# Kernel tuning notes

Measured on AMD Instinct MI355X. Metric: run time of the kernel, lower is better.

Reference implementation:

```python
import jax, jax.numpy as jnp
import numpy as np

N, H, W, PD, HID, NH = 2, 64, 64, 16, 128, 4
EPS = 1e-5


def _bn(x, g, b):
    # training-mode BatchNorm over (N, H, W) with biased variance, channels last
    m = jnp.mean(x, axis=(0, 1, 2), keepdims=True)
    v = jnp.var(x, axis=(0, 1, 2), keepdims=True)
    return (x - m) * jax.lax.rsqrt(v + EPS) * g + b


def _mha(x, in_w, in_b, out_w, out_b, nh):
    # torch nn.MultiheadAttention (batch_first) with packed qkv in_proj
    B, S, E = x.shape
    hd = E // nh
    q, k, v = jnp.split(x @ in_w.T + in_b, 3, axis=-1)
    def heads(t):
        return t.reshape(B, S, nh, hd).transpose(0, 2, 1, 3)  # B,nh,S,hd
    q, k, v = heads(q), heads(k), heads(v)
    a = jax.nn.softmax(jnp.einsum('bnqd,bnkd->bnqk', q, k) / np.float32(np.sqrt(hd)), axis=-1)
    o = jnp.einsum('bnqk,bnkd->bnqd', a, v).transpose(0, 2, 1, 3).reshape(B, S, E)
    return o @ out_w.T + out_b


def setup_inputs():
    key = jax.random.key(0)
    ks = jax.random.split(key, 32)
    def r(i, shape, s=0.1):
        return jax.random.normal(ks[i], shape, dtype=jnp.float32) * s
    mask = (jnp.arange(W) % 2) == 0  # alternating columns kept, M = W//2
    return {
        'kspace': jax.random.normal(ks[0], (N, 2, H, W), dtype=jnp.float32),
        'mask': mask,
        'pre_conv_w': r(1, (PD, 2), 0.5), 'pre_conv_b': r(2, (PD,)),
        'pre_pe_H': r(3, (H, PD)), 'pre_pe_W': r(4, (W, PD)),
        'res_conv1_w': r(5, (PD, PD), 0.2), 'res_conv1_b': r(6, (PD,)),
        'res_bn1_g': 1.0 + r(7, (PD,)), 'res_bn1_b': r(8, (PD,)),
        'res_conv2_w': r(9, (PD, PD), 0.2), 'res_conv2_b': r(10, (PD,)),
        'res_bn2_g': 1.0 + r(11, (PD,)), 'res_bn2_b': r(12, (PD,)),
        'proj_w': r(13, (HID, PD), 0.2), 'proj_b': r(14, (HID,)),
        'enc_in_w': r(15, (3 * HID, HID), 0.08), 'enc_in_b': r(16, (3 * HID,)),
        'enc_out_w': r(17, (HID, HID), 0.08), 'enc_out_b': r(18, (HID,)),
        'dec_pe_H': r(19, (H, HID)), 'dec_pe_W': r(20, (W, HID)),
        'dec_in_w': r(21, (3 * HID, HID), 0.08), 'dec_in_b': r(22, (3 * HID,)),
        'dec_out_w': r(23, (HID, HID), 0.08), 'dec_out_b': r(24, (HID,)),
        'masked_token': r(25, (HID,), 1.0),
        'post_w': r(26, (2, HID), 0.1), 'post_b': r(27, (2,)),
    }


def reference(kspace, mask, pre_conv_w, pre_conv_b, pre_pe_H, pre_pe_W,
              res_conv1_w, res_conv1_b, res_bn1_g, res_bn1_b,
              res_conv2_w, res_conv2_b, res_bn2_g, res_bn2_b,
              proj_w, proj_b, enc_in_w, enc_in_b, enc_out_w, enc_out_b,
              dec_pe_H, dec_pe_W, dec_in_w, dec_in_b, dec_out_w, dec_out_b,
              masked_token, post_w, post_b):
    cols = np.nonzero(np.asarray(mask))[0]  # static sampled columns
    M = cols.shape[0]
    # gather valid columns; channels last: [N, H, M, 2]
    x = kspace.transpose(0, 2, 3, 1)[:, :, cols, :]
    h = x @ pre_conv_w.T + pre_conv_b  # 1x1 conv -> [N, H, M, PD]
    h = h + (pre_pe_H[:, None, :] + pre_pe_W[cols][None, :, :])
    # PixelwiseConstantChannelResNet (1 layer)
    r1 = jax.nn.relu(_bn(h @ res_conv1_w.T + res_conv1_b, res_bn1_g, res_bn1_b))
    r2 = jax.nn.relu(_bn(r1 @ res_conv2_w.T + res_conv2_b, res_bn2_g, res_bn2_b))
    h = jax.nn.relu(h + r2)
    h = h @ proj_w.T + proj_b  # [N, H, M, HID]
    enc = _mha(h.reshape(N, H * M, HID), enc_in_w, enc_in_b, enc_out_w, enc_out_b, NH)
    # scatter: fill unmasked positions with masked_token, masked with encoder output
    dec = jnp.broadcast_to(masked_token, (N, H, W, HID))
    dec = dec.at[:, :, cols, :].set(enc.reshape(N, H, M, HID))
    dec = dec + (dec_pe_H[:, None, :] + dec_pe_W[None, :, :])
    dec = _mha(dec.reshape(N, H * W, HID), dec_in_w, dec_in_b, dec_out_w, dec_out_b, NH)
    out = dec.reshape(N, H, W, HID) @ post_w.T + post_b  # [N, H, W, 2]
    return out.transpose(0, 3, 1, 2)  # [N, 2, H, W]
```

## Files before the change

kernel.cpp:

```cpp
#include <hip/hip_runtime.h>
#include <math.h>

#define N_ 2
#define H_ 64
#define W_ 64
#define M_ 32
#define PD_ 16
#define HID_ 128
#define NH_ 4
#define HD_ 32
#define S_ENC 2048
#define S_DEC 4096
#define EPS_ 1e-5f
#define SCALE_ 0.17677669529663687f
#define SCALE2_ (0.17677669529663687f * 1.4426950408889634f)

#define OFF_H     0
#define OFF_T1    65536
#define OFF_T2    131072
#define OFF_STAT  196608
#define OFF_WP    196672
#define OFF_BP    202816
#define OFF_QBF   203264
#define OFF_KBF   727552
#define OFF_VTBF  1251840
#define OFF_ATTBF 1776128
#define OFF_XBF2  2300416
#define OFF_WBF   2824704

#define WOFF_ENC_OUT 0
#define WOFF_DEC_IN  16384
#define WOFF_DEC_OUT 65536

#define IB_MF   2048
#define IB_WC   320
#define IB_WP   24
#define IB_BP   2
#define IB_TOT  (IB_MF + IB_WC + IB_WP + IB_BP + 1)

typedef short bf16x8 __attribute__((ext_vector_type(8)));
typedef short bf16x4 __attribute__((ext_vector_type(4)));
typedef float f32x4 __attribute__((ext_vector_type(4)));

__device__ __forceinline__ short f2bf(float f) {
  union { float f; unsigned u; } v; v.f = f;
  unsigned r = v.u + 0x7FFFu + ((v.u >> 16) & 1u);
  return (short)(r >> 16);
}

__global__ void k_init(const float* __restrict__ eow, const float* __restrict__ dw,
                       const float* __restrict__ dow, const float* __restrict__ mt,
                       const float* __restrict__ peH, const float* __restrict__ peW,
                       const float* __restrict__ ew, const float* __restrict__ pw,
                       const float* __restrict__ pb, const float* __restrict__ eib,
                       short* __restrict__ wbf, short* __restrict__ xdec,
                       float* __restrict__ wp, float* __restrict__ bp,
                       float* __restrict__ stat) {
  int blk = blockIdx.x, tid = threadIdx.x;
  if (blk < IB_MF) {
    int idx = blk * 256 + tid;
    int j = idx & 127;
    int widx = (idx >> 7) & 31;
    int hh = (idx >> 12) & 63;
    int b = idx >> 18;
    int w = 2 * widx + 1;
    xdec[((size_t)(b * 4096 + hh * 64 + w)) * 128 + j] =
        f2bf(mt[j] + peH[hh * 128 + j] + peW[w * 128 + j]);
  } else if (blk < IB_MF + IB_WC) {
    int idx = (blk - IB_MF) * 256 + tid;
    float v;
    if (idx < 16384) v = eow[idx];
    else if (idx < 65536) v = dw[idx - 16384];
    else v = dow[idx - 65536];
    wbf[idx] = f2bf(v);
  } else if (blk < IB_MF + IB_WC + IB_WP) {
    int e = (blk - IB_MF - IB_WC) * 256 + tid;
    int row = e >> 4, k = e & 15;
    float a = 0.f;
    for (int j = 0; j < 128; j++) a = fmaf(ew[row * 128 + j], pw[j * 16 + k], a);
    wp[e] = a;
  } else if (blk < IB_MF + IB_WC + IB_WP + IB_BP) {
    int row = (blk - IB_MF - IB_WC - IB_WP) * 256 + tid;
    if (row < 384) {
      float a = eib[row];
      for (int j = 0; j < 128; j++) a = fmaf(ew[row * 128 + j], pb[j], a);
      bp[row] = a;
    }
  } else {
    if (tid < 64) stat[tid] = 0.f;
  }
}

__global__ void k_prelin_stats(const float* __restrict__ ks, const float* __restrict__ pcw,
                               const float* __restrict__ pcb, const float* __restrict__ peH,
                               const float* __restrict__ peW, const float* __restrict__ w1,
                               const float* __restrict__ b1, float* __restrict__ h,
                               float* __restrict__ t1, float* __restrict__ stat) {
  int tid = threadIdx.x;
  int pos = blockIdx.x * 256 + tid;
  int m = pos & 31, hh = (pos >> 5) & 63, b = pos >> 11;
  int w = 2 * m;
  float x0 = ks[((b * 2 + 0) * H_ + hh) * W_ + w];
  float x1 = ks[((b * 2 + 1) * H_ + hh) * W_ + w];
  float hv[16], tv[16];
#pragma unroll
  for (int c = 0; c < 16; c++)
    hv[c] = x0 * pcw[c * 2] + x1 * pcw[c * 2 + 1] + pcb[c]
            + peH[hh * PD_ + c] + peW[w * PD_ + c];
#pragma unroll
  for (int c = 0; c < 16; c += 4)
    *(float4*)&h[pos * 16 + c] = make_float4(hv[c], hv[c + 1], hv[c + 2], hv[c + 3]);
#pragma unroll
  for (int c = 0; c < 16; c++) {
    float a = b1[c];
#pragma unroll
    for (int k = 0; k < 16; k++) a = fmaf(hv[k], w1[c * 16 + k], a);
    tv[c] = a;
    t1[pos * 16 + c] = a;
  }
  __shared__ float tl[256][17];
#pragma unroll
  for (int c = 0; c < 16; c++) tl[tid][c] = tv[c];
  __syncthreads();
  int c = tid & 15, g = tid >> 4;
  float s = 0.f, s2 = 0.f;
#pragma unroll
  for (int r = 0; r < 16; r++) {
    float v = tl[g * 16 + r][c];
    s += v; s2 += v * v;
  }
  __shared__ float ps[16][16], ps2[16][16];
  ps[g][c] = s; ps2[g][c] = s2;
  __syncthreads();
  if (tid < 16) {
    float S = 0.f, S2 = 0.f;
#pragma unroll
    for (int g2 = 0; g2 < 16; g2++) { S += ps[g2][tid]; S2 += ps2[g2][tid]; }
    atomicAdd(&stat[tid], S);
    atomicAdd(&stat[16 + tid], S2);
  }
}

__global__ void k_bnlin_stats(const float* __restrict__ t1, const float* __restrict__ stat,
                              const float* __restrict__ g1, const float* __restrict__ bb1,
                              const float* __restrict__ w2, const float* __restrict__ b2,
                              float* __restrict__ t2, float* __restrict__ statw) {
  int tid = threadIdx.x;
  int pos = blockIdx.x * 256 + tid;
  const float inv = 1.f / 4096.f;
  float r[16];
#pragma unroll
  for (int k = 0; k < 16; k++) {
    float mu = stat[k] * inv;
    float var = stat[16 + k] * inv - mu * mu;
    float v = (t1[pos * 16 + k] - mu) * rsqrtf(var + EPS_) * g1[k] + bb1[k];
    r[k] = fmaxf(v, 0.f);
  }
  float tv[16];
#pragma unroll
  for (int c = 0; c < 16; c++) {
    float a = b2[c];
#pragma unroll
    for (int k = 0; k < 16; k++) a = fmaf(r[k], w2[c * 16 + k], a);
    tv[c] = a;
    t2[pos * 16 + c] = a;
  }
  __shared__ float tl[256][17];
#pragma unroll
  for (int c = 0; c < 16; c++) tl[tid][c] = tv[c];
  __syncthreads();
  int c = tid & 15, g = tid >> 4;
  float s = 0.f, s2 = 0.f;
#pragma unroll
  for (int rr = 0; rr < 16; rr++) {
    float v = tl[g * 16 + rr][c];
    s += v; s2 += v * v;
  }
  __shared__ float ps[16][16], ps2[16][16];
  ps[g][c] = s; ps2[g][c] = s2;
  __syncthreads();
  if (tid < 16) {
    float S = 0.f, S2 = 0.f;
#pragma unroll
    for (int g2 = 0; g2 < 16; g2++) { S += ps[g2][tid]; S2 += ps2[g2][tid]; }
    atomicAdd(&statw[32 + tid], S);
    atomicAdd(&statw[48 + tid], S2);
  }
}

__global__ __launch_bounds__(256)
void k_fqkv_enc(const float* __restrict__ h, const float* __restrict__ t2,
                const float* __restrict__ stat, const float* __restrict__ g2,
                const float* __restrict__ bb2, const float* __restrict__ wp,
                const float* __restrict__ bp, short* __restrict__ qbf,
                short* __restrict__ kbf, short* __restrict__ vtbf) {
  int tid = threadIdx.x;
  int p0 = blockIdx.x * 32;
  __shared__ float hf[32][20];
  const float inv = 1.f / 4096.f;
#pragma unroll
  for (int i = 0; i < 2; i++) {
    int idx = tid * 2 + i;
    int lp = idx >> 4, c = idx & 15;
    int pos = p0 + lp;
    float mu = stat[32 + c] * inv;
    float var = stat[48 + c] * inv - mu * mu;
    float v = (t2[pos * 16 + c] - mu) * rsqrtf(var + EPS_) * g2[c] + bb2[c];
    v = fmaxf(v, 0.f);
    hf[lp][c] = fmaxf(h[pos * 16 + c] + v, 0.f);
  }
  __syncthreads();
  int bb = p0 >> 11;
  int sbase = p0 & 2047;
  {
    int col = tid;
    float wc[16];
#pragma unroll
    for (int k = 0; k < 16; k += 4) *(float4*)&wc[k] = *(const float4*)&wp[col * 16 + k];
    float bpv = bp[col];
    int isQ = (col < 128);
    int c2 = isQ ? col : (col - 128);
    int hd = c2 >> 5, d = c2 & 31;
    short* dst = isQ ? qbf : kbf;
    float sc = isQ ? SCALE2_ : 1.f;
    size_t rowb = ((size_t)(bb * 4 + hd) * S_ENC + sbase) * 32 + d;
    for (int lp = 0; lp < 32; lp++) {
      float a = bpv;
#pragma unroll
      for (int k = 0; k < 16; k++) a = fmaf(hf[lp][k], wc[k], a);
      dst[rowb + (size_t)lp * 32] = f2bf(a * sc);
    }
  }
  if (tid < 128) {
    int col = 256 + tid;
    float wc[16];
#pragma unroll
    for (int k = 0; k < 16; k += 4) *(float4*)&wc[k] = *(const float4*)&wp[col * 16 + k];
    float bpv = bp[col];
    int c2 = tid;
    int hd = c2 >> 5, d = c2 & 31;
    size_t rowb = ((size_t)(bb * 4 + hd) * 32 + d) * S_ENC + sbase;
    for (int lp4 = 0; lp4 < 32; lp4 += 4) {
      bf16x4 pk;
#pragma unroll
      for (int r = 0; r < 4; r++) {
        float a = bpv;
#pragma unroll
        for (int k = 0; k < 16; k++) a = fmaf(hf[lp4 + r][k], wc[k], a);
        pk[r] = f2bf(a);
      }
      *(bf16x4*)&vtbf[rowb + lp4] = pk;
    }
  }
}

#define MGEMM_STAGE_AND_FRAGS                                                   \
  __shared__ short As[64 * 128];                                                \
  __shared__ short Wl[64 * 128];                                                \
  int tid = threadIdx.x;                                                        \
  _Pragma("unroll")                                                             \
  for (int i = 0; i < 4; i++) {                                                 \
    int idx = i * 256 + tid;                                                    \
    int row = idx >> 4, c = idx & 15, slot = c ^ (row & 7);                     \
    *(bf16x8*)&As[row * 128 + slot * 8] =                                       \
        *(const bf16x8*)&abf[(size_t)(rb + row) * 128 + c * 8];                 \
    *(bf16x8*)&Wl[row * 128 + slot * 8] =                                       \
        *(const bf16x8*)&wbf[(size_t)(ob + row) * 128 + c * 8];                 \
  }                                                                             \
  __syncthreads();                                                              \
  int lane = tid & 63, wv = tid >> 6;                                           \
  int l15 = lane & 15, quad = lane >> 4;                                        \
  int m0 = wv * 16;                                                             \
  f32x4 acc[4];                                                                 \
  acc[0] = acc[1] = acc[2] = acc[3] = (f32x4){0.f, 0.f, 0.f, 0.f};              \
  _Pragma("unroll")                                                             \
  for (int kk = 0; kk < 4; kk++) {                                              \
    int sl = ((kk * 4 + quad) ^ (l15 & 7)) * 8;                                 \
    bf16x8 af = *(const bf16x8*)&As[(m0 + l15) * 128 + sl];                     \
    _Pragma("unroll")                                                           \
    for (int nt = 0; nt < 4; nt++) {                                            \
      bf16x8 wf = *(const bf16x8*)&Wl[(nt * 16 + l15) * 128 + sl];              \
      acc[nt] = __builtin_amdgcn_mfma_f32_16x16x32_bf16(af, wf, acc[nt], 0, 0, 0); \
    }                                                                           \
  }

__global__ __launch_bounds__(256)
void k_mgemm_qkv_dec(const short* __restrict__ abf, const short* __restrict__ wbf,
                     const float* __restrict__ bias, short* __restrict__ qbf,
                     short* __restrict__ kbf, short* __restrict__ vtbf) {
  const int S = 4096;
  int rb = blockIdx.x * 64, ob = blockIdx.y * 64;
  MGEMM_STAGE_AND_FRAGS
#pragma unroll
  for (int nt = 0; nt < 4; nt++) {
    int col = ob + nt * 16 + l15;
    float bv = bias[col];
    if (ob < 128) {
      int hd = col >> 5, d = col & 31;
#pragma unroll
      for (int r = 0; r < 4; r++) {
        int grow = rb + m0 + quad * 4 + r;
        int bb = grow >> 12, s = grow & (S - 1);
        qbf[((size_t)(bb * 4 + hd) * S + s) * 32 + d] =
            f2bf((acc[nt][r] + bv) * SCALE2_);
      }
    } else if (ob < 256) {
      int c2 = col - 128, hd = c2 >> 5, d = c2 & 31;
#pragma unroll
      for (int r = 0; r < 4; r++) {
        int grow = rb + m0 + quad * 4 + r;
        int bb = grow >> 12, s = grow & (S - 1);
        kbf[((size_t)(bb * 4 + hd) * S + s) * 32 + d] = f2bf(acc[nt][r] + bv);
      }
    } else {
      int c2 = col - 256, hd = c2 >> 5, d = c2 & 31;
      int grow0 = rb + m0 + quad * 4;
      int bb = grow0 >> 12, s0 = grow0 & (S - 1);
      bf16x4 pk;
#pragma unroll
      for (int r = 0; r < 4; r++) pk[r] = f2bf(acc[nt][r] + bv);
      *(bf16x4*)&vtbf[((size_t)(bb * 4 + hd) * 32 + d) * S + s0] = pk;
    }
  }
}

__global__ __launch_bounds__(256)
void k_mgemm_out_enc(const short* __restrict__ abf, const short* __restrict__ wbf,
                     const float* __restrict__ bias, const float* __restrict__ peH,
                     const float* __restrict__ peW, short* __restrict__ xdec) {
  int rb = blockIdx.x * 64, ob = blockIdx.y * 64;
  MGEMM_STAGE_AND_FRAGS
#pragma unroll
  for (int nt = 0; nt < 4; nt++) {
    int col = ob + nt * 16 + l15;
    float bv = bias[col];
#pragma unroll
    for (int r = 0; r < 4; r++) {
      int grow = rb + m0 + quad * 4 + r;
      int bb = grow >> 11, rem = grow & 2047;
      int hhh = rem >> 5, m = rem & 31, w = 2 * m;
      xdec[((size_t)(bb * 4096 + hhh * 64 + w)) * 128 + col] =
          f2bf(acc[nt][r] + bv + peH[hhh * 128 + col] + peW[w * 128 + col]);
    }
  }
}

__global__ __launch_bounds__(256)
void k_mgemm_out_post(const short* __restrict__ abf, const short* __restrict__ wbf,
                      const float* __restrict__ bias, const float* __restrict__ pw,
                      const float* __restrict__ pb, float* __restrict__ outp) {
  int rb = blockIdx.x * 64;
  __shared__ short As[64 * 128];
  __shared__ short Wl[128 * 128];
  int tid = threadIdx.x;
#pragma unroll
  for (int i = 0; i < 4; i++) {
    int idx = i * 256 + tid;
    int row = idx >> 4, c = idx & 15, slot = c ^ (row & 7);
    *(bf16x8*)&As[row * 128 + slot * 8] =
        *(const bf16x8*)&abf[(size_t)(rb + row) * 128 + c * 8];
  }
#pragma unroll
  for (int i = 0; i < 8; i++) {
    int idx = i * 256 + tid;
    int row = idx >> 4, c = idx & 15, slot = c ^ (row & 7);
    *(bf16x8*)&Wl[row * 128 + slot * 8] =
        *(const bf16x8*)&wbf[(size_t)row * 128 + c * 8];
  }
  __syncthreads();
  int lane = tid & 63, wv = tid >> 6;
  int l15 = lane & 15, quad = lane >> 4;
  int m0 = wv * 16;
  f32x4 acc[8];
#pragma unroll
  for (int nt = 0; nt < 8; nt++) acc[nt] = (f32x4){0.f, 0.f, 0.f, 0.f};
#pragma unroll
  for (int kk = 0; kk < 4; kk++) {
    int sl = ((kk * 4 + quad) ^ (l15 & 7)) * 8;
    bf16x8 af = *(const bf16x8*)&As[(m0 + l15) * 128 + sl];
#pragma unroll
    for (int nt = 0; nt < 8; nt++) {
      bf16x8 wf = *(const bf16x8*)&Wl[(nt * 16 + l15) * 128 + sl];
      acc[nt] = __builtin_amdgcn_mfma_f32_16x16x32_bf16(af, wf, acc[nt], 0, 0, 0);
    }
  }
  float bv[8], pw0[8], pw1[8];
#pragma unroll
  for (int nt = 0; nt < 8; nt++) {
    int col = nt * 16 + l15;
    bv[nt] = bias[col];
    pw0[nt] = pw[col];
    pw1[nt] = pw[128 + col];
  }
  float pb0 = pb[0], pb1 = pb[1];
#pragma unroll
  for (int r = 0; r < 4; r++) {
    float pc0 = 0.f, pc1 = 0.f;
#pragma unroll
    for (int nt = 0; nt < 8; nt++) {
      float yv = acc[nt][r] + bv[nt];
      pc0 = fmaf(yv, pw0[nt], pc0);
      pc1 = fmaf(yv, pw1[nt], pc1);
    }
    pc0 += __shfl_xor(pc0, 1); pc0 += __shfl_xor(pc0, 2);
    pc0 += __shfl_xor(pc0, 4); pc0 += __shfl_xor(pc0, 8);
    pc1 += __shfl_xor(pc1, 1); pc1 += __shfl_xor(pc1, 2);
    pc1 += __shfl_xor(pc1, 4); pc1 += __shfl_xor(pc1, 8);
    if (l15 == 0) {
      int grow = rb + m0 + quad * 4 + r;
      int bb = grow >> 12, hw = grow & 4095;
      outp[(size_t)(bb * 2 + 0) * 4096 + hw] = pc0 + pb0;
      outp[(size_t)(bb * 2 + 1) * 4096 + hw] = pc1 + pb1;
    }
  }
}

template <int S>
__global__ __launch_bounds__(1024)
__attribute__((amdgpu_waves_per_eu(8)))
void k_attn15(const short* __restrict__ qbf, const short* __restrict__ kbf,
              const short* __restrict__ vtbf, short* __restrict__ outb) {
  __shared__ __align__(16) char smem[65536];
  short* kb4 = (short*)smem;
  short* vt4 = (short*)(smem + 32768);
  float* abuf = (float*)smem;
  float* lb   = (float*)(smem + 24576);

  int qt = blockIdx.x, hh = blockIdx.y, b = blockIdx.z;
  int tid = threadIdx.x;
  int lane = tid & 63;
  int wv = tid >> 6;
  int qtr = wv >> 2;
  int wv4 = wv & 3;
  int l15 = lane & 15, quad = lane >> 4;
  int t256 = tid & 255;

  int bh = b * NH_ + hh;
  const short* kg = kbf + (size_t)bh * S * 32;
  const short* vg = vtbf + (size_t)bh * 32 * S;
  short* kbh = kb4 + qtr * 2048;
  short* vth = vt4 + qtr * 2048;

  bf16x8 qf = *(const bf16x8*)&qbf[((size_t)bh * S + qt * 64 + wv4 * 16 + l15) * 32
                                   + quad * 8];

  f32x4 acc[2];
  acc[0] = (f32x4){0.f, 0.f, 0.f, 0.f};
  acc[1] = (f32x4){0.f, 0.f, 0.f, 0.f};
  f32x4 accl = (f32x4){0.f, 0.f, 0.f, 0.f};
  const short ONEB = (short)0x3F80;
  const bf16x8 ones = {ONEB, ONEB, ONEB, ONEB, ONEB, ONEB, ONEB, ONEB};

  int srowK = t256 >> 2, schK = t256 & 3;
  int slotK = schK ^ ((srowK >> 1) & 3);
  int srowV = t256 >> 3, sslV = t256 & 7;
  int sgV = sslV ^ (srowV & 7);
  int gbV = ((sgV >> 2) << 5) + ((sgV & 3) << 2);

  int kq0 = qtr * (S / 4);
  int kxor = (l15 >> 1) & 3;
  int vsl = l15 & 7;

  const short* kgp = kg + (size_t)(kq0 + srowK) * 32 + schK * 8;
  const short* vgp0 = vg + (size_t)srowV * S + kq0 + gbV;
  const short* vgp1 = vgp0 + 16;
  short* kdst = kbh + srowK * 32 + slotK * 8;
  short* vdst = vth + srowV * 64 + sslV * 8;

  bf16x8 krg = *(const bf16x8*)kgp;
  bf16x4 vr0 = *(const bf16x4*)vgp0;
  bf16x4 vr1 = *(const bf16x4*)vgp1;

  constexpr int NIT = S / 256;
  for (int it = 0; it < NIT; ++it) {
    int co = (it & 1) << 13;
    *(bf16x8*)(kdst + co) = krg;
    *(bf16x8*)(vdst + co) = __builtin_shufflevector(vr0, vr1, 0, 1, 2, 3, 4, 5, 6, 7);
    if (it + 1 < NIT) {
      kgp += 64 * 32;
      vgp0 += 64;
      vgp1 += 64;
      krg = *(const bf16x8*)kgp;
      vr0 = *(const bf16x4*)vgp0;
      vr1 = *(const bf16x4*)vgp1;
    }
    asm volatile("s_waitcnt lgkmcnt(0)" ::: "memory");
    __builtin_amdgcn_s_barrier();
    asm volatile("" ::: "memory");

    const short* kbhc = kbh + co;
    const short* vthc = vth + co;

    f32x4 s[4];
#pragma unroll
    for (int t = 0; t < 4; t++) {
      bf16x8 kf = *(const bf16x8*)&kbhc[(t * 16 + l15) * 32 + ((quad ^ kxor) * 8)];
      s[t] = __builtin_amdgcn_mfma_f32_16x16x32_bf16(
          kf, qf, (f32x4){0.f, 0.f, 0.f, 0.f}, 0, 0, 0);
    }

    float pe[4][4];
#pragma unroll
    for (int t = 0; t < 4; t++) {
      pe[t][0] = __builtin_exp2f(s[t][0]);
      pe[t][1] = __builtin_exp2f(s[t][1]);
      pe[t][2] = __builtin_exp2f(s[t][2]);
      pe[t][3] = __builtin_exp2f(s[t][3]);
    }

#pragma unroll
    for (int kh = 0; kh < 2; kh++) {
      union { unsigned u[4]; bf16x8 v; } pf;
      asm("v_cvt_pk_bf16_f32 %0, %1, %2"
          : "=v"(pf.u[0]) : "v"(pe[2 * kh][0]), "v"(pe[2 * kh][1]));
      asm("v_cvt_pk_bf16_f32 %0, %1, %2"
          : "=v"(pf.u[1]) : "v"(pe[2 * kh][2]), "v"(pe[2 * kh][3]));
      asm("v_cvt_pk_bf16_f32 %0, %1, %2"
          : "=v"(pf.u[2]) : "v"(pe[2 * kh + 1][0]), "v"(pe[2 * kh + 1][1]));
      asm("v_cvt_pk_bf16_f32 %0, %1, %2"
          : "=v"(pf.u[3]) : "v"(pe[2 * kh + 1][2]), "v"(pe[2 * kh + 1][3]));
#pragma unroll
      for (int nt = 0; nt < 2; nt++) {
        bf16x8 vf = *(const bf16x8*)&vthc[(nt * 16 + l15) * 64
                                          + (((kh * 4 + quad) ^ vsl) * 8)];
        acc[nt] = __builtin_amdgcn_mfma_f32_16x16x32_bf16(vf, pf.v, acc[nt], 0, 0, 0);
      }
      accl = __builtin_amdgcn_mfma_f32_16x16x32_bf16(ones, pf.v, accl, 0, 0, 0);
    }
  }

  float lpart = accl[0];

  __syncthreads();
  if (qtr > 0) {
#pragma unroll
    for (int nt = 0; nt < 2; nt++)
#pragma unroll
      for (int r = 0; r < 4; r++)
        abuf[(qtr - 1) * 2048 + wv4 * 512 + (nt * 16 + quad * 4 + r) * 16 + l15] =
            acc[nt][r];
    if (quad == 0) lb[(qtr - 1) * 64 + wv4 * 16 + l15] = lpart;
  }
  __syncthreads();
  if (qtr == 0) {
    int li = wv4 * 16 + l15;
    float ltot = lpart + lb[li] + lb[64 + li] + lb[128 + li];
    float inv = 1.f / ltot;
    int base = wv4 * 512;
    short* op = outb + ((size_t)(b * S + qt * 64 + wv4 * 16 + l15)) * 128 + hh * 32;
#pragma unroll
    for (int nt = 0; nt < 2; nt++) {
      bf16x4 pk;
#pragma unroll
      for (int r = 0; r < 4; r++) {
        int d = nt * 16 + quad * 4 + r;
        float v = acc[nt][r] + abuf[base + d * 16 + l15]
                + abuf[2048 + base + d * 16 + l15]
                + abuf[4096 + base + d * 16 + l15];
        pk[r] = f2bf(v * inv);
      }
      *(bf16x4*)&op[nt * 16 + quad * 4] = pk;
    }
  }
}

extern "C" void kernel_launch(void* const* d_in, const int* in_sizes, int n_in,
                              void* d_out, int out_size, void* d_ws, size_t ws_size,
                              hipStream_t stream) {
  const float* ks        = (const float*)d_in[0];
  const float* pre_conv_w = (const float*)d_in[2];
  const float* pre_conv_b = (const float*)d_in[3];
  const float* pre_pe_H   = (const float*)d_in[4];
  const float* pre_pe_W   = (const float*)d_in[5];
  const float* w1  = (const float*)d_in[6];
  const float* b1  = (const float*)d_in[7];
  const float* g1  = (const float*)d_in[8];
  const float* bb1 = (const float*)d_in[9];
  const float* w2  = (const float*)d_in[10];
  const float* b2  = (const float*)d_in[11];
  const float* g2  = (const float*)d_in[12];
  const float* bb2 = (const float*)d_in[13];
  const float* proj_w = (const float*)d_in[14];
  const float* proj_b = (const float*)d_in[15];
  const float* enc_in_w  = (const float*)d_in[16];
  const float* enc_in_b  = (const float*)d_in[17];
  const float* enc_out_w = (const float*)d_in[18];
  const float* enc_out_b = (const float*)d_in[19];
  const float* dec_pe_H  = (const float*)d_in[20];
  const float* dec_pe_W  = (const float*)d_in[21];
  const float* dec_in_w  = (const float*)d_in[22];
  const float* dec_in_b  = (const float*)d_in[23];
  const float* dec_out_w = (const float*)d_in[24];
  const float* dec_out_b = (const float*)d_in[25];
  const float* masked_token = (const float*)d_in[26];
  const float* post_w = (const float*)d_in[27];
  const float* post_b = (const float*)d_in[28];
  float* out = (float*)d_out;

  float* ws    = (float*)d_ws;
  float* h     = ws + OFF_H;
  float* t1    = ws + OFF_T1;
  float* t2    = ws + OFF_T2;
  float* stat  = ws + OFF_STAT;
  float* wp    = ws + OFF_WP;
  float* bp    = ws + OFF_BP;
  short* qbf   = (short*)(ws + OFF_QBF);
  short* kbfb  = (short*)(ws + OFF_KBF);
  short* vtbfb = (short*)(ws + OFF_VTBF);
  short* attbf = (short*)(ws + OFF_ATTBF);
  short* xbf2  = (short*)(ws + OFF_XBF2);
  short* wbf   = (short*)(ws + OFF_WBF);

  k_init<<<IB_TOT, 256, 0, stream>>>(enc_out_w, dec_in_w, dec_out_w, masked_token,
                                     dec_pe_H, dec_pe_W, enc_in_w, proj_w, proj_b,
                                     enc_in_b, wbf, xbf2, wp, bp, stat);
  k_prelin_stats<<<16, 256, 0, stream>>>(ks, pre_conv_w, pre_conv_b, pre_pe_H,
                                         pre_pe_W, w1, b1, h, t1, stat);
  k_bnlin_stats<<<16, 256, 0, stream>>>(t1, stat, g1, bb1, w2, b2, t2, stat);
  k_fqkv_enc<<<128, 256, 0, stream>>>(h, t2, stat, g2, bb2, wp, bp,
                                      qbf, kbfb, vtbfb);
  k_attn15<S_ENC><<<dim3(S_ENC / 64, NH_, N_), 1024, 0, stream>>>(qbf, kbfb, vtbfb, attbf);
  k_mgemm_out_enc<<<dim3(S_ENC * N_ / 64, 2), 256, 0, stream>>>(
      attbf, wbf + WOFF_ENC_OUT, enc_out_b, dec_pe_H, dec_pe_W, xbf2);
  k_mgemm_qkv_dec<<<dim3(S_DEC * N_ / 64, 6), 256, 0, stream>>>(
      xbf2, wbf + WOFF_DEC_IN, dec_in_b, qbf, kbfb, vtbfb);
  k_attn15<S_DEC><<<dim3(S_DEC / 64, NH_, N_), 1024, 0, stream>>>(qbf, kbfb, vtbfb, attbf);
  k_mgemm_out_post<<<S_DEC * N_ / 64, 256, 0, stream>>>(
      attbf, wbf + WOFF_DEC_OUT, dec_out_b, post_w, post_b, out);
}
```

Baseline: 202.9 us.

## Add 128-query-tile attention kernel for decoder to double K/V reuse

Adds a new attention kernel in which each wave handles 32 queries (two 16-row MFMA groups) instead of 16, so each block covers 128 queries. Every K/V tile staged in shared memory is reused across twice as many queries, and the grid for decoder attention is halved. The cost is more accumulator registers per wave, which may lower occupancy and leaves fewer blocks in flight. The encoder keeps the old kernel.

```diff
diff --git a/kernel.cpp b/kernel.cpp
--- a/kernel.cpp
+++ b/kernel.cpp
@@ -564,6 +564,182 @@
   }
 }
 
+template <int S>
+__global__ __launch_bounds__(1024, 4)
+void k_attn16(const short* __restrict__ qbf, const short* __restrict__ kbf,
+              const short* __restrict__ vtbf, short* __restrict__ outb) {
+  __shared__ __align__(16) char smem[65536];
+  short* kb4 = (short*)smem;
+  short* vt4 = (short*)(smem + 32768);
+  float* abuf = (float*)smem;
+  float* lb   = (float*)(smem + 49152);
+
+  int qt = blockIdx.x, hh = blockIdx.y, b = blockIdx.z;
+  int tid = threadIdx.x;
+  int lane = tid & 63;
+  int wv = tid >> 6;
+  int qtr = wv >> 2;
+  int qsub = wv & 3;
+  int l15 = lane & 15, quad = lane >> 4;
+  int t256 = tid & 255;
+
+  int bh = b * NH_ + hh;
+  const short* kg = kbf + (size_t)bh * S * 32;
+  const short* vg = vtbf + (size_t)bh * 32 * S;
+  short* kbh = kb4 + qtr * 2048;
+  short* vth = vt4 + qtr * 2048;
+
+  const short* qrow = &qbf[((size_t)bh * S + qt * 128 + qsub * 32 + l15) * 32
+                           + quad * 8];
+  bf16x8 qf0 = *(const bf16x8*)qrow;
+  bf16x8 qf1 = *(const bf16x8*)(qrow + 16 * 32);
+
+  f32x4 acc00 = {0.f,0.f,0.f,0.f}, acc01 = {0.f,0.f,0.f,0.f};
+  f32x4 acc10 = {0.f,0.f,0.f,0.f}, acc11 = {0.f,0.f,0.f,0.f};
+  f32x4 accl0 = {0.f,0.f,0.f,0.f}, accl1 = {0.f,0.f,0.f,0.f};
+  const short ONEB = (short)0x3F80;
+  const bf16x8 ones = {ONEB, ONEB, ONEB, ONEB, ONEB, ONEB, ONEB, ONEB};
+
+  int srowK = t256 >> 2, schK = t256 & 3;
+  int slotK = schK ^ ((srowK >> 1) & 3);
+  int srowV = t256 >> 3, sslV = t256 & 7;
+  int sgV = sslV ^ (srowV & 7);
+  int gbV = ((sgV >> 2) << 5) + ((sgV & 3) << 2);
+
+  int kq0 = qtr * (S / 4);
+  int kxor = (l15 >> 1) & 3;
+  int vsl = l15 & 7;
+
+  const short* kgp = kg + (size_t)(kq0 + srowK) * 32 + schK * 8;
+  const short* vgp0 = vg + (size_t)srowV * S + kq0 + gbV;
+  const short* vgp1 = vgp0 + 16;
+  short* kdst = kbh + srowK * 32 + slotK * 8;
+  short* vdst = vth + srowV * 64 + sslV * 8;
+
+  bf16x8 krg = *(const bf16x8*)kgp;
+  bf16x4 vr0 = *(const bf16x4*)vgp0;
+  bf16x4 vr1 = *(const bf16x4*)vgp1;
+
+  constexpr int NIT = S / 256;
+  for (int it = 0; it < NIT; ++it) {
+    int co = (it & 1) << 13;
+    *(bf16x8*)(kdst + co) = krg;
+    *(bf16x8*)(vdst + co) = __builtin_shufflevector(vr0, vr1, 0, 1, 2, 3, 4, 5, 6, 7);
+    if (it + 1 < NIT) {
+      kgp += 64 * 32;
+      vgp0 += 64;
+      vgp1 += 64;
+      krg = *(const bf16x8*)kgp;
+      vr0 = *(const bf16x4*)vgp0;
+      vr1 = *(const bf16x4*)vgp1;
+    }
+    asm volatile("s_waitcnt lgkmcnt(0)" ::: "memory");
+    __builtin_amdgcn_s_barrier();
+    asm volatile("" ::: "memory");
+
+    const short* kbhc = kbh + co;
+    const short* vthc = vth + co;
+
+    f32x4 s0[4], s1[4];
+#pragma unroll
+    for (int t = 0; t < 4; t++) {
+      bf16x8 kf = *(const bf16x8*)&kbhc[(t * 16 + l15) * 32 + ((quad ^ kxor) * 8)];
+      s0[t] = __builtin_amdgcn_mfma_f32_16x16x32_bf16(
+          kf, qf0, (f32x4){0.f, 0.f, 0.f, 0.f}, 0, 0, 0);
+      s1[t] = __builtin_amdgcn_mfma_f32_16x16x32_bf16(
+          kf, qf1, (f32x4){0.f, 0.f, 0.f, 0.f}, 0, 0, 0);
+    }
+
+#pragma unroll
+    for (int kh = 0; kh < 2; kh++) {
+      bf16x8 vfa = *(const bf16x8*)&vthc[(0 * 16 + l15) * 64
+                                         + (((kh * 4 + quad) ^ vsl) * 8)];
+      bf16x8 vfb = *(const bf16x8*)&vthc[(1 * 16 + l15) * 64
+                                         + (((kh * 4 + quad) ^ vsl) * 8)];
+      {
+        float pa0 = __builtin_exp2f(s0[2 * kh][0]);
+        float pa1 = __builtin_exp2f(s0[2 * kh][1]);
+        float pa2 = __builtin_exp2f(s0[2 * kh][2]);
+        float pa3 = __builtin_exp2f(s0[2 * kh][3]);
+        float pb0v = __builtin_exp2f(s0[2 * kh + 1][0]);
+        float pb1v = __builtin_exp2f(s0[2 * kh + 1][1]);
+        float pb2v = __builtin_exp2f(s0[2 * kh + 1][2]);
+        float pb3v = __builtin_exp2f(s0[2 * kh + 1][3]);
+        union { unsigned u[4]; bf16x8 v; } pf;
+        asm("v_cvt_pk_bf16_f32 %0, %1, %2" : "=v"(pf.u[0]) : "v"(pa0), "v"(pa1));
+        asm("v_cvt_pk_bf16_f32 %0, %1, %2" : "=v"(pf.u[1]) : "v"(pa2), "v"(pa3));
+        asm("v_cvt_pk_bf16_f32 %0, %1, %2" : "=v"(pf.u[2]) : "v"(pb0v), "v"(pb1v));
+        asm("v_cvt_pk_bf16_f32 %0, %1, %2" : "=v"(pf.u[3]) : "v"(pb2v), "v"(pb3v));
+        acc00 = __builtin_amdgcn_mfma_f32_16x16x32_bf16(vfa, pf.v, acc00, 0, 0, 0);
+        acc01 = __builtin_amdgcn_mfma_f32_16x16x32_bf16(vfb, pf.v, acc01, 0, 0, 0);
+        accl0 = __builtin_amdgcn_mfma_f32_16x16x32_bf16(ones, pf.v, accl0, 0, 0, 0);
+      }
+      {
+        float pa0 = __builtin_exp2f(s1[2 * kh][0]);
+        float pa1 = __builtin_exp2f(s1[2 * kh][1]);
+        float pa2 = __builtin_exp2f(s1[2 * kh][2]);
+        float pa3 = __builtin_exp2f(s1[2 * kh][3]);
+        float pb0v = __builtin_exp2f(s1[2 * kh + 1][0]);
+        float pb1v = __builtin_exp2f(s1[2 * kh + 1][1]);
+        float pb2v = __builtin_exp2f(s1[2 * kh + 1][2]);
+        float pb3v = __builtin_exp2f(s1[2 * kh + 1][3]);
+        union { unsigned u[4]; bf16x8 v; } pf;
+        asm("v_cvt_pk_bf16_f32 %0, %1, %2" : "=v"(pf.u[0]) : "v"(pa0), "v"(pa1));
+        asm("v_cvt_pk_bf16_f32 %0, %1, %2" : "=v"(pf.u[1]) : "v"(pa2), "v"(pa3));
+        asm("v_cvt_pk_bf16_f32 %0, %1, %2" : "=v"(pf.u[2]) : "v"(pb0v), "v"(pb1v));
+        asm("v_cvt_pk_bf16_f32 %0, %1, %2" : "=v"(pf.u[3]) : "v"(pb2v), "v"(pb3v));
+        acc10 = __builtin_amdgcn_mfma_f32_16x16x32_bf16(vfa, pf.v, acc10, 0, 0, 0);
+        acc11 = __builtin_amdgcn_mfma_f32_16x16x32_bf16(vfb, pf.v, acc11, 0, 0, 0);
+        accl1 = __builtin_amdgcn_mfma_f32_16x16x32_bf16(ones, pf.v, accl1, 0, 0, 0);
+      }
+    }
+  }
+
+  __syncthreads();
+  if (qtr > 0) {
+    float* ab = abuf + (qtr - 1) * 4096 + (qsub * 2) * 512;
+#pragma unroll
+    for (int r = 0; r < 4; r++) {
+      ab[(0 * 16 + quad * 4 + r) * 16 + l15] = acc00[r];
+      ab[(1 * 16 + quad * 4 + r) * 16 + l15] = acc01[r];
+      ab[512 + (0 * 16 + quad * 4 + r) * 16 + l15] = acc10[r];
+      ab[512 + (1 * 16 + quad * 4 + r) * 16 + l15] = acc11[r];
+    }
+    if (quad == 0) {
+      lb[(qtr - 1) * 128 + qsub * 32 + l15] = accl0[0];
+      lb[(qtr - 1) * 128 + qsub * 32 + 16 + l15] = accl1[0];
+    }
+  }
+  __syncthreads();
+  if (qtr == 0) {
+#pragma unroll
+    for (int j = 0; j < 2; j++) {
+      int li = qsub * 32 + j * 16 + l15;
+      float lpart = (j == 0) ? accl0[0] : accl1[0];
+      float ltot = lpart + lb[li] + lb[128 + li] + lb[256 + li];
+      float inv = 1.f / ltot;
+      int base = (qsub * 2 + j) * 512;
+      f32x4 a0 = (j == 0) ? acc00 : acc10;
+      f32x4 a1 = (j == 0) ? acc01 : acc11;
+      short* op = outb + ((size_t)(b * S + qt * 128 + li)) * 128 + hh * 32;
+#pragma unroll
+      for (int nt = 0; nt < 2; nt++) {
+        bf16x4 pk;
+#pragma unroll
+        for (int r = 0; r < 4; r++) {
+          int d = nt * 16 + quad * 4 + r;
+          float v = ((nt == 0) ? a0[r] : a1[r])
+                  + abuf[base + d * 16 + l15]
+                  + abuf[4096 + base + d * 16 + l15]
+                  + abuf[8192 + base + d * 16 + l15];
+          pk[r] = f2bf(v * inv);
+        }
+        *(bf16x4*)&op[nt * 16 + quad * 4] = pk;
+      }
+    }
+  }
+}
+
 extern "C" void kernel_launch(void* const* d_in, const int* in_sizes, int n_in,
                               void* d_out, int out_size, void* d_ws, size_t ws_size,
                               hipStream_t stream) {
@@ -624,7 +800,7 @@
       attbf, wbf + WOFF_ENC_OUT, enc_out_b, dec_pe_H, dec_pe_W, xbf2);
   k_mgemm_qkv_dec<<<dim3(S_DEC * N_ / 64, 6), 256, 0, stream>>>(
       xbf2, wbf + WOFF_DEC_IN, dec_in_b, qbf, kbfb, vtbfb);
-  k_attn15<S_DEC><<<dim3(S_DEC / 64, NH_, N_), 1024, 0, stream>>>(qbf, kbfb, vtbfb, attbf);
+  k_attn16<S_DEC><<<dim3(S_DEC / 128, NH_, N_), 1024, 0, stream>>>(qbf, kbfb, vtbfb, attbf);
   k_mgemm_out_post<<<S_DEC * N_ / 64, 256, 0, stream>>>(
       attbf, wbf + WOFF_DEC_OUT, dec_out_b, post_w, post_b, out);
 }
```

Result: faster. 196.1 us (median of 3 runs) (-3.4%).
